# Kernel tuning notes

Hardware: AMD Instinct MI355X
Metric: run time of the kernel (lower is better)

Reference implementation:

```python
import jax, jax.numpy as jnp
import numpy as np

B, T, I, H, O = 4096, 512, 15, 64, 1


def setup_inputs() -> dict:
    key = jax.random.key(0)
    ks = jax.random.split(key, 7)
    s_rnn = 1.0 / np.sqrt(H)  # torch nn.RNN init scale
    s_fc = 1.0 / np.sqrt(H)   # torch nn.Linear init scale (fan_in = H)
    u = lambda k, shape, s: jax.random.uniform(k, shape, jnp.float32, -s, s)
    return {
        "x": jax.random.normal(ks[0], (B, T, I), jnp.float32),
        "W_ih": u(ks[1], (H, I), s_rnn),
        "W_hh": u(ks[2], (H, H), s_rnn),
        "b_ih": u(ks[3], (H,), s_rnn),
        "b_hh": u(ks[4], (H,), s_rnn),
        "fc_w": u(ks[5], (O, H), s_fc),
        "fc_b": u(ks[6], (O,), s_fc),
    }


def reference(x, W_ih, W_hh, b_ih, b_hh, fc_w, fc_b):
    # Precompute input projection for all timesteps in one GEMM: [B, T, H]
    xp = jnp.einsum("bti,hi->bth", x, W_ih) + b_ih + b_hh

    def step(h, xt):  # h: [B, H], xt: [B, H]
        h_new = jnp.tanh(xt + h @ W_hh.T)
        return h_new, None

    h0 = jnp.zeros((x.shape[0], W_hh.shape[0]), x.dtype)
    hT, _ = jax.lax.scan(step, h0, jnp.swapaxes(xp, 0, 1))  # scan over time
    # last-step linear head: [B, O]
    return hT @ fc_w.T + fc_b
```

## Files before the change

kernel.cpp:

```cpp
#include <hip/hip_runtime.h>


#define T_STEPS 512
#define I_DIM 15
#define BPW 16
#define RING 16

typedef _Float16 half8 __attribute__((ext_vector_type(8)));
typedef __attribute__((ext_vector_type(4))) float float4v;
typedef __attribute__((ext_vector_type(4))) unsigned int uint4v;

union H8U { half8 h; uint4v u; };

__device__ __forceinline__ unsigned pkh(float a, float b) {
    union { _Float16 h; unsigned short u; } A, B;
    A.h = (_Float16)a;
    B.h = (_Float16)b;
    return (unsigned)A.u | ((unsigned)B.u << 16);
}
__device__ __forceinline__ unsigned pkz(float a, float b) {
    auto r = __builtin_amdgcn_cvt_pkrtz(a, b);
    unsigned u;
    __builtin_memcpy(&u, &r, 4);
    return u;
}

__global__ __launch_bounds__(256, 1) void rnn_fused(
    const float* __restrict__ x,
    const float* __restrict__ W_ih,
    const float* __restrict__ W_hh,
    const float* __restrict__ b_ih,
    const float* __restrict__ b_hh,
    const float* __restrict__ fc_w,
    const float* __restrict__ fc_b,
    float* __restrict__ out)
{
    __shared__ uint4v xring[RING][32];
    __shared__ uint2  hx[2][4][64];
    __shared__ float  psum[4][16];

    const int tid  = threadIdx.x;
    const int wave = tid >> 6;
    const int lane = tid & 63;
    const int q = lane >> 4;
    const int n = lane & 15;
    const int b0 = blockIdx.x * BPW;
    const int jt = wave;
    const float K = 2.8853900817779268f;

    half8 whf[3];
    float4v cbv;
    float fcwv[4];
    const int jcol = 32*(jt>>1) + 8*(n>>2) + 4*(jt&1) + (n&3);
    #pragma unroll
    for (int c = 0; c < 3; c++) {
        #pragma unroll
        for (int e = 0; e < 8; e++) {
            const int k = c*32 + q*8 + e;
            float w = 0.f;
            if (k < 64)      w = W_hh[jcol*64 + k] * K;
            else if (k < 79) w = W_ih[jcol*15 + (k - 64)] * K;
            whf[c][e] = (_Float16)w;
        }
    }
    #pragma unroll
    for (int r = 0; r < 4; r++) {
        const int jr = 32*(jt>>1) + 8*q + 4*(jt&1) + r;
        cbv[r]  = K * (b_ih[jr] + b_hh[jr]);
        fcwv[r] = fc_w[jr];
    }

    const float* xrow = x + (size_t)(b0 + n) * (T_STEPS * I_DIM);

    if (lane < 16) {
        #pragma unroll
        for (int j = 0; j < 2; j++) {
            const int s = wave + 4*j;
            float v[16];
            __builtin_memcpy(v, xrow + (size_t)s * I_DIM, 60);
            v[15] = 0.f;
            xring[s & (RING-1)][n] = (uint4v){ pkh(v[0],v[1]), pkh(v[2],v[3]),
                                               pkh(v[4],v[5]), pkh(v[6],v[7]) };
            xring[s & (RING-1)][n + 16] = (uint4v){ pkh(v[8],v[9]),  pkh(v[10],v[11]),
                                                    pkh(v[12],v[13]), pkh(v[14],v[15]) };
        }
    }
    hx[1][wave][lane] = uint2{0u, 0u};
    float rowbuf[15];
    if (lane < 16)
        __builtin_memcpy(rowbuf, xrow + (size_t)(wave + 8) * I_DIM, 60);

    asm volatile("s_waitcnt lgkmcnt(0)\n\ts_barrier" ::: "memory");

    uint4v xf = xring[0][lane & 31];
    float4v acc;
    float hfin[4];

    for (int it = 0; it < T_STEPS / 4; ++it) {
        #pragma unroll
        for (int u = 0; u < 4; ++u) {
            const int t = it * 4 + u;
            const uint2 h0a = hx[(t+1)&1][0][lane];
            const uint2 h0b = hx[(t+1)&1][1][lane];
            const uint2 h1a = hx[(t+1)&1][2][lane];
            const uint2 h1b = hx[(t+1)&1][3][lane];
            const uint4v xfn = xring[(t+1)&(RING-1)][lane & 31];

            H8U xb_; xb_.u = xf;
            acc = __builtin_amdgcn_mfma_f32_16x16x32_f16(whf[2], xb_.h, cbv, 0, 0, 0);

            if (wave == u) {
                if (lane < 16) {
                    const int s = t + 8;
                    xring[s & (RING-1)][n] = (uint4v){ pkh(rowbuf[0],rowbuf[1]), pkh(rowbuf[2],rowbuf[3]),
                                                       pkh(rowbuf[4],rowbuf[5]), pkh(rowbuf[6],rowbuf[7]) };
                    xring[s & (RING-1)][n + 16] = (uint4v){ pkh(rowbuf[8],rowbuf[9]),   pkh(rowbuf[10],rowbuf[11]),
                                                            pkh(rowbuf[12],rowbuf[13]), pkh(rowbuf[14], 0.f) };
                    int tl = t + 12; if (tl > T_STEPS - 1) tl = T_STEPS - 1;
                    __builtin_memcpy(rowbuf, xrow + (size_t)tl * I_DIM, 60);
                }
            }

            H8U hh0; hh0.u = (uint4v){h0a.x, h0a.y, h0b.x, h0b.y};
            acc = __builtin_amdgcn_mfma_f32_16x16x32_f16(whf[0], hh0.h, acc, 0, 0, 0);
            H8U hh1; hh1.u = (uint4v){h1a.x, h1a.y, h1b.x, h1b.y};
            acc = __builtin_amdgcn_mfma_f32_16x16x32_f16(whf[1], hh1.h, acc, 0, 0, 0);

            #pragma unroll
            for (int r = 0; r < 4; r++) {
                float ex = __builtin_amdgcn_exp2f(acc[r]);
                hfin[r] = __builtin_fmaf(-2.f, __builtin_amdgcn_rcpf(ex + 1.f), 1.f);
            }
            uint2 hp; hp.x = pkz(hfin[0], hfin[1]); hp.y = pkz(hfin[2], hfin[3]);
            hx[t&1][wave][lane] = hp;

            asm volatile("s_waitcnt lgkmcnt(0)\n\ts_barrier" ::: "memory");
            xf = xfn;
        }
    }

    float s = 0.f;
    #pragma unroll
    for (int r = 0; r < 4; r++) s = __builtin_fmaf(hfin[r], fcwv[r], s);
    s += __shfl_xor(s, 16, 64);
    s += __shfl_xor(s, 32, 64);
    if (lane < 16) psum[wave][n] = s;
    __syncthreads();
    if (tid < 16)
        out[b0 + tid] = psum[0][tid] + psum[1][tid] + psum[2][tid]
                      + psum[3][tid] + fc_b[0];
}

extern "C" void kernel_launch(void* const* d_in, const int* in_sizes, int n_in,
                              void* d_out, int out_size, void* d_ws, size_t ws_size,
                              hipStream_t stream) {
    const float* x    = (const float*)d_in[0];
    const float* W_ih = (const float*)d_in[1];
    const float* W_hh = (const float*)d_in[2];
    const float* b_ih = (const float*)d_in[3];
    const float* b_hh = (const float*)d_in[4];
    const float* fc_w = (const float*)d_in[5];
    const float* fc_b = (const float*)d_in[6];
    float* out = (float*)d_out;

    rnn_fused<<<4096 / BPW, 256, 0, stream>>>(x, W_ih, W_hh, b_ih, b_hh,
                                              fc_w, fc_b, out);
}
```

Before: 272.5 us.

## Replace LDS x ring with per-lane register prefetch and precomputed input MFMA

Result: slower. 389.4 us (+42.9%).

```diff
diff --git a/kernel.cpp b/kernel.cpp
--- a/kernel.cpp
+++ b/kernel.cpp
@@ -4,7 +4,6 @@
 #define T_STEPS 512
 #define I_DIM 15
 #define BPW 16
-#define RING 16
 
 typedef _Float16 half8 __attribute__((ext_vector_type(8)));
 typedef __attribute__((ext_vector_type(4))) float float4v;
@@ -24,6 +23,17 @@
     __builtin_memcpy(&u, &r, 4);
     return u;
 }
+__device__ __forceinline__ uint4v packx(const float* v, int g) {
+    float a0 = g ? v[1] : v[0];
+    float a1 = g ? v[2] : v[1];
+    float a2 = g ? v[3] : v[2];
+    float a3 = g ? v[4] : v[3];
+    float a4 = g ? v[5] : v[4];
+    float a5 = g ? v[6] : v[5];
+    float a6 = g ? v[7] : v[6];
+    float a7 = g ? 0.f  : v[7];
+    return (uint4v){ pkh(a0, a1), pkh(a2, a3), pkh(a4, a5), pkh(a6, a7) };
+}
 
 __global__ __launch_bounds__(256, 1) void rnn_fused(
     const float* __restrict__ x,
@@ -35,15 +45,15 @@
     const float* __restrict__ fc_b,
     float* __restrict__ out)
 {
-    __shared__ uint4v xring[RING][32];
-    __shared__ uint2  hx[2][4][64];
-    __shared__ float  psum[4][16];
+    __shared__ uint2 hx[2][4][64];
+    __shared__ float psum[4][16];
 
     const int tid  = threadIdx.x;
     const int wave = tid >> 6;
     const int lane = tid & 63;
     const int q = lane >> 4;
     const int n = lane & 15;
+    const int g = q & 1;
     const int b0 = blockIdx.x * BPW;
     const int jt = wave;
     const float K = 2.8853900817779268f;
@@ -70,72 +80,64 @@
         fcwv[r] = fc_w[jr];
     }
 
-    const float* xrow = x + (size_t)(b0 + n) * (T_STEPS * I_DIM);
+    const float* xl = x + (size_t)(b0 + n) * (T_STEPS * I_DIM) + g * 7;
 
-    if (lane < 16) {
-        #pragma unroll
-        for (int j = 0; j < 2; j++) {
-            const int s = wave + 4*j;
-            float v[16];
-            __builtin_memcpy(v, xrow + (size_t)s * I_DIM, 60);
-            v[15] = 0.f;
-            xring[s & (RING-1)][n] = (uint4v){ pkh(v[0],v[1]), pkh(v[2],v[3]),
-                                               pkh(v[4],v[5]), pkh(v[6],v[7]) };
-            xring[s & (RING-1)][n + 16] = (uint4v){ pkh(v[8],v[9]),  pkh(v[10],v[11]),
-                                                    pkh(v[12],v[13]), pkh(v[14],v[15]) };
-        }
-    }
+    float xs[4][8];
+    #pragma unroll
+    for (int s = 0; s < 4; ++s)
+        __builtin_memcpy(xs[s], xl + (size_t)s * I_DIM, 32);
+
     hx[1][wave][lane] = uint2{0u, 0u};
-    float rowbuf[15];
-    if (lane < 16)
-        __builtin_memcpy(rowbuf, xrow + (size_t)(wave + 8) * I_DIM, 60);
+
+    H8U xf0; xf0.u = packx(xs[0], g);
+    float4v accx = __builtin_amdgcn_mfma_f32_16x16x32_f16(whf[2], xf0.h, cbv, 0, 0, 0);
 
     asm volatile("s_waitcnt lgkmcnt(0)\n\ts_barrier" ::: "memory");
 
-    uint4v xf = xring[0][lane & 31];
     float4v acc;
     float hfin[4];
 
+    #pragma unroll 1
     for (int it = 0; it < T_STEPS / 4; ++it) {
         #pragma unroll
         for (int u = 0; u < 4; ++u) {
             const int t = it * 4 + u;
-            const uint2 h0a = hx[(t+1)&1][0][lane];
-            const uint2 h0b = hx[(t+1)&1][1][lane];
-            const uint2 h1a = hx[(t+1)&1][2][lane];
-            const uint2 h1b = hx[(t+1)&1][3][lane];
-            const uint4v xfn = xring[(t+1)&(RING-1)][lane & 31];
+            const int pr = (u + 1) & 1;
+            const uint2 h0a = hx[pr][0][lane];
+            const uint2 h0b = hx[pr][1][lane];
+            const uint2 h1a = hx[pr][2][lane];
+            const uint2 h1b = hx[pr][3][lane];
 
-            H8U xb_; xb_.u = xf;
-            acc = __builtin_amdgcn_mfma_f32_16x16x32_f16(whf[2], xb_.h, cbv, 0, 0, 0);
+            acc = accx;
 
-            if (wave == u) {
-                if (lane < 16) {
-                    const int s = t + 8;
-                    xring[s & (RING-1)][n] = (uint4v){ pkh(rowbuf[0],rowbuf[1]), pkh(rowbuf[2],rowbuf[3]),
-                                                       pkh(rowbuf[4],rowbuf[5]), pkh(rowbuf[6],rowbuf[7]) };
-                    xring[s & (RING-1)][n + 16] = (uint4v){ pkh(rowbuf[8],rowbuf[9]),   pkh(rowbuf[10],rowbuf[11]),
-                                                            pkh(rowbuf[12],rowbuf[13]), pkh(rowbuf[14], 0.f) };
-                    int tl = t + 12; if (tl > T_STEPS - 1) tl = T_STEPS - 1;
-                    __builtin_memcpy(rowbuf, xrow + (size_t)tl * I_DIM, 60);
-                }
-            }
+            H8U xfn; xfn.u = packx(xs[(u + 1) & 3], g);
+            accx = __builtin_amdgcn_mfma_f32_16x16x32_f16(whf[2], xfn.h, cbv, 0, 0, 0);
+            int tl = t + 4; if (tl > T_STEPS - 1) tl = T_STEPS - 1;
+            __builtin_memcpy(xs[u], xl + (size_t)tl * I_DIM, 32);
 
             H8U hh0; hh0.u = (uint4v){h0a.x, h0a.y, h0b.x, h0b.y};
             acc = __builtin_amdgcn_mfma_f32_16x16x32_f16(whf[0], hh0.h, acc, 0, 0, 0);
             H8U hh1; hh1.u = (uint4v){h1a.x, h1a.y, h1b.x, h1b.y};
             acc = __builtin_amdgcn_mfma_f32_16x16x32_f16(whf[1], hh1.h, acc, 0, 0, 0);
 
-            #pragma unroll
-            for (int r = 0; r < 4; r++) {
-                float ex = __builtin_amdgcn_exp2f(acc[r]);
-                hfin[r] = __builtin_fmaf(-2.f, __builtin_amdgcn_rcpf(ex + 1.f), 1.f);
+            {
+                float E0 = __builtin_amdgcn_exp2f(acc[0]) + 1.f;
+                float E1 = __builtin_amdgcn_exp2f(acc[1]) + 1.f;
+                float R0 = __builtin_amdgcn_rcpf(E0 * E1);
+                float m0 = -2.f * R0;
+                hfin[0] = __builtin_fmaf(E1, m0, 1.f);
+                hfin[1] = __builtin_fmaf(E0, m0, 1.f);
+                float E2 = __builtin_amdgcn_exp2f(acc[2]) + 1.f;
+                float E3 = __builtin_amdgcn_exp2f(acc[3]) + 1.f;
+                float R2 = __builtin_amdgcn_rcpf(E2 * E3);
+                float m2 = -2.f * R2;
+                hfin[2] = __builtin_fmaf(E3, m2, 1.f);
+                hfin[3] = __builtin_fmaf(E2, m2, 1.f);
             }
             uint2 hp; hp.x = pkz(hfin[0], hfin[1]); hp.y = pkz(hfin[2], hfin[3]);
-            hx[t&1][wave][lane] = hp;
+            hx[u & 1][wave][lane] = hp;
 
             asm volatile("s_waitcnt lgkmcnt(0)\n\ts_barrier" ::: "memory");
-            xf = xfn;
         }
     }
 
```
